# Kernel optimization log

Hardware: AMD Instinct MI355X
Metric: run time of the kernel (lower is better)

The kernel has to match this reference:

```python
import jax, jax.numpy as jnp
import numpy as np

B, S, HID = 2, 2048, 1024
NH, NKV, HD = 16, 8, 128
EPS = 1e-6
THETA = 1.0e6
NEG = -1e9

def _rope_tables():
    inv_freq = 1.0 / (THETA ** (np.arange(0, HD, 2, dtype=np.float32) / HD))  # [HD/2]
    pos = np.arange(S, dtype=np.float32)
    freqs = np.outer(pos, inv_freq)                      # [S, HD/2]
    emb = np.concatenate([freqs, freqs], axis=-1)        # [S, HD]
    cos = np.broadcast_to(np.cos(emb), (B, S, HD)).copy()
    sin = np.broadcast_to(np.sin(emb), (B, S, HD)).copy()
    return jnp.asarray(cos), jnp.asarray(sin)

def setup_inputs() -> dict:
    key = jax.random.key(0)
    ks = jax.random.split(key, 8)
    hidden_states = jax.random.normal(ks[0], (B, S, HID), jnp.float32)
    cos, sin = _rope_tables()
    # additive causal mask [B,1,S,S]
    causal = jnp.triu(jnp.full((S, S), NEG, jnp.float32), k=1)
    attention_mask = jnp.broadcast_to(causal[None, None], (B, 1, S, S))
    std = 0.02
    Wq = jax.random.normal(ks[1], (NH * HD, HID), jnp.float32) * std
    Wk = jax.random.normal(ks[2], (NKV * HD, HID), jnp.float32) * std
    Wv = jax.random.normal(ks[3], (NKV * HD, HID), jnp.float32) * std
    Wo = jax.random.normal(ks[4], (HID, NH * HD), jnp.float32) * std
    q_norm_w = jnp.ones((HD,), jnp.float32)
    k_norm_w = jnp.ones((HD,), jnp.float32)
    return {"hidden_states": hidden_states, "cos": cos, "sin": sin,
            "attention_mask": attention_mask, "Wq": Wq, "Wk": Wk, "Wv": Wv,
            "Wo": Wo, "q_norm_w": q_norm_w, "k_norm_w": k_norm_w}

def _rms_norm(x, w):
    var = jnp.mean(jnp.square(x), axis=-1, keepdims=True)
    return x * jax.lax.rsqrt(var + EPS) * w

def _rotate_half(x):
    x1, x2 = jnp.split(x, 2, axis=-1)
    return jnp.concatenate([-x2, x1], axis=-1)

def reference(hidden_states, cos, sin, attention_mask, Wq, Wk, Wv, Wo, q_norm_w, k_norm_w):
    # projections: [B,S,heads,HD] -> [B,heads,S,HD]
    q = jnp.einsum('bsh,dh->bsd', hidden_states, Wq).reshape(B, S, NH, HD)
    k = jnp.einsum('bsh,dh->bsd', hidden_states, Wk).reshape(B, S, NKV, HD)
    v = jnp.einsum('bsh,dh->bsd', hidden_states, Wv).reshape(B, S, NKV, HD)
    q = jnp.transpose(_rms_norm(q, q_norm_w), (0, 2, 1, 3))
    k = jnp.transpose(_rms_norm(k, k_norm_w), (0, 2, 1, 3))
    v = jnp.transpose(v, (0, 2, 1, 3))
    c = cos[:, None]  # [B,1,S,HD]
    s = sin[:, None]
    q = q * c + _rotate_half(q) * s
    k = k * c + _rotate_half(k) * s
    # repeat kv heads: NKV -> NH
    n_rep = NH // NKV
    k = jnp.repeat(k, n_rep, axis=1)
    v = jnp.repeat(v, n_rep, axis=1)
    scaling = HD ** -0.5
    scores = jnp.einsum('bhqd,bhkd->bhqk', q, k) * scaling
    scores = scores + attention_mask
    probs = jax.nn.softmax(scores.astype(jnp.float32), axis=-1).astype(q.dtype)
    out = jnp.einsum('bhqk,bhkd->bhqd', probs, v)
    out = jnp.transpose(out, (0, 2, 1, 3)).reshape(B, S, NH * HD)
    return jnp.einsum('bsd,hd->bsh', out, Wo)
```

## Files before the change

### kernel.cpp

```cpp
#include <hip/hip_runtime.h>
#include <hip/hip_fp16.h>


typedef _Float16 f16;
typedef __attribute__((ext_vector_type(8))) _Float16 f16x8;
typedef __attribute__((ext_vector_type(4))) _Float16 f16x4;
typedef __attribute__((ext_vector_type(4))) float f32x4;

__constant__ const float kEps = 1e-6f;
__constant__ const float kScaleL2 = 0.1275179120685481f;

#define ASYNC_LD16(gp, lp)                                              \
  __builtin_amdgcn_global_load_lds(                                     \
      (const __attribute__((address_space(1))) void*)(gp),              \
      (__attribute__((address_space(3))) void*)(uint32_t)(uintptr_t)(lp), 16, 0, 0)

__global__ __launch_bounds__(256) void cast_all(
    const float* __restrict__ h, const float* __restrict__ wq,
    const float* __restrict__ wk, const float* __restrict__ wv,
    const float* __restrict__ wo, f16* __restrict__ hb,
    f16* __restrict__ wqkv, f16* __restrict__ wob) {
  const int idx = blockIdx.x * 256 + threadIdx.x;
  const float* src;
  f16* dst;
  int base;
  if (idx < 1048576) { src = h;  dst = hb;                  base = 0; }
  else if (idx < 1572864) { src = wq; dst = wqkv;               base = 1048576; }
  else if (idx < 1835008) { src = wk; dst = wqkv + 2048 * 1024; base = 1572864; }
  else if (idx < 2097152) { src = wv; dst = wqkv + 3072 * 1024; base = 1835008; }
  else { src = wo; dst = wob; base = 2097152; }
  const int i = (idx - base) * 4;
  f32x4 v = *reinterpret_cast<const f32x4*>(src + i);
  f16x4 o;
  o.x = (f16)v.x; o.y = (f16)v.y; o.z = (f16)v.z; o.w = (f16)v.w;
  *reinterpret_cast<f16x4*>(dst + i) = o;
}

__global__ __launch_bounds__(256) void gemm_bt_h(const f16* __restrict__ A,
                                                 const f16* __restrict__ Bm,
                                                 f16* __restrict__ C,
                                                 int M, int N, int K) {
  __shared__ __align__(16) f16 As[128][64];
  __shared__ __align__(16) f16 Bs[128][64];
  const int tid = threadIdx.x;
  const int lane = tid & 63;
  const int wave = tid >> 6;
  const int cl = lane & 15;
  const int quad = lane >> 4;
  const int wm = (wave >> 1) * 64;
  const int wn = (wave & 1) * 64;
  const int tm = blockIdx.y * 128;
  const int tn = blockIdx.x * 128;
  const int r0 = tid >> 3;
  const int csw = ((tid & 7) ^ (r0 & 7)) * 8;

  const f16* Ab = A + (size_t)(tm + r0) * K + csw;
  const f16* Bb = Bm + (size_t)(tn + r0) * K + csw;
  char* Al = (char*)As + wave * 1024;
  char* Bl = (char*)Bs + wave * 1024;

  f32x4 acc[4][4] = {};

  for (int k0 = 0; k0 < K; k0 += 64) {
#pragma unroll
    for (int c = 0; c < 4; ++c) {
      ASYNC_LD16(Ab + (size_t)(c * 32) * K + k0, Al + c * 4096);
      ASYNC_LD16(Bb + (size_t)(c * 32) * K + k0, Bl + c * 4096);
    }
    __syncthreads();
#pragma unroll
    for (int kk = 0; kk < 2; ++kk) {
      f16x8 af[4], bf[4];
#pragma unroll
      for (int mi = 0; mi < 4; ++mi)
        af[mi] = *reinterpret_cast<const f16x8*>(
            &As[wm + mi * 16 + cl][((kk * 4 + quad) ^ (cl & 7)) * 8]);
#pragma unroll
      for (int ni = 0; ni < 4; ++ni)
        bf[ni] = *reinterpret_cast<const f16x8*>(
            &Bs[wn + ni * 16 + cl][((kk * 4 + quad) ^ (cl & 7)) * 8]);
#pragma unroll
      for (int mi = 0; mi < 4; ++mi)
#pragma unroll
        for (int ni = 0; ni < 4; ++ni)
          acc[mi][ni] =
              __builtin_amdgcn_mfma_f32_16x16x32_f16(af[mi], bf[ni], acc[mi][ni], 0, 0, 0);
    }
    __syncthreads();
  }
#pragma unroll
  for (int mi = 0; mi < 4; ++mi)
#pragma unroll
    for (int ni = 0; ni < 4; ++ni)
#pragma unroll
      for (int r = 0; r < 4; ++r)
        C[(size_t)(tm + wm + mi * 16 + quad * 4 + r) * N + tn + wn + ni * 16 + cl] =
            (f16)acc[mi][ni][r];
}

__global__ __launch_bounds__(256) void gemm_bt64(const f16* __restrict__ A,
                                                 const f16* __restrict__ Bm,
                                                 float* __restrict__ C,
                                                 int M, int N, int K) {
  __shared__ __align__(16) f16 As[64][64];
  __shared__ __align__(16) f16 Bs[128][64];
  const int tid = threadIdx.x;
  const int lane = tid & 63;
  const int wave = tid >> 6;
  const int cl = lane & 15;
  const int quad = lane >> 4;
  const int wm = (wave >> 1) * 32;
  const int wn = (wave & 1) * 64;
  const int tm = blockIdx.y * 64;
  const int tn = blockIdx.x * 128;
  const int r0 = tid >> 3;
  const int csw = ((tid & 7) ^ (r0 & 7)) * 8;

  const f16* Ab = A + (size_t)(tm + r0) * K + csw;
  const f16* Bb = Bm + (size_t)(tn + r0) * K + csw;
  char* Al = (char*)As + wave * 1024;
  char* Bl = (char*)Bs + wave * 1024;

  f32x4 acc[2][4] = {};

  for (int k0 = 0; k0 < K; k0 += 64) {
#pragma unroll
    for (int c = 0; c < 2; ++c)
      ASYNC_LD16(Ab + (size_t)(c * 32) * K + k0, Al + c * 4096);
#pragma unroll
    for (int c = 0; c < 4; ++c)
      ASYNC_LD16(Bb + (size_t)(c * 32) * K + k0, Bl + c * 4096);
    __syncthreads();
#pragma unroll
    for (int kk = 0; kk < 2; ++kk) {
      f16x8 af[2], bf[4];
#pragma unroll
      for (int mi = 0; mi < 2; ++mi)
        af[mi] = *reinterpret_cast<const f16x8*>(
            &As[wm + mi * 16 + cl][((kk * 4 + quad) ^ (cl & 7)) * 8]);
#pragma unroll
      for (int ni = 0; ni < 4; ++ni)
        bf[ni] = *reinterpret_cast<const f16x8*>(
            &Bs[wn + ni * 16 + cl][((kk * 4 + quad) ^ (cl & 7)) * 8]);
#pragma unroll
      for (int mi = 0; mi < 2; ++mi)
#pragma unroll
        for (int ni = 0; ni < 4; ++ni)
          acc[mi][ni] =
              __builtin_amdgcn_mfma_f32_16x16x32_f16(af[mi], bf[ni], acc[mi][ni], 0, 0, 0);
    }
    __syncthreads();
  }
#pragma unroll
  for (int mi = 0; mi < 2; ++mi)
#pragma unroll
    for (int ni = 0; ni < 4; ++ni)
#pragma unroll
      for (int r = 0; r < 4; ++r)
        C[(size_t)(tm + wm + mi * 16 + quad * 4 + r) * N + tn + wn + ni * 16 + cl] =
            acc[mi][ni][r];
}

__global__ __launch_bounds__(256) void rope_norm(
    const f16* __restrict__ qkvh,
    const float* __restrict__ cosT, const float* __restrict__ sinT,
    const float* __restrict__ qw, const float* __restrict__ kw,
    f16* __restrict__ qt, f16* __restrict__ kt) {
  const int gw = blockIdx.x * 4 + (threadIdx.x >> 6);
  const int lane = threadIdx.x & 63;
  const int head = gw % 24;
  const int bs = gw / 24;
  const bool isq = head < 16;
  const f16* src = qkvh + (size_t)bs * 4096 +
                   (isq ? head * 128 : 2048 + (head - 16) * 128);
  const float x1 = (float)src[lane];
  const float x2 = (float)src[lane + 64];
  float ss = x1 * x1 + x2 * x2;
#pragma unroll
  for (int off = 32; off >= 1; off >>= 1) ss += __shfl_xor(ss, off);
  const float rms = rsqrtf(ss * (1.0f / 128.0f) + kEps);
  const float* w = isq ? qw : kw;
  const float n1 = x1 * rms * w[lane];
  const float n2 = x2 * rms * w[lane + 64];
  const float* cb = cosT + (size_t)bs * 128;
  const float* sb = sinT + (size_t)bs * 128;
  const float o1 = n1 * cb[lane] - n2 * sb[lane];
  const float o2 = n2 * cb[lane + 64] + n1 * sb[lane + 64];
  const int b = bs >> 11;
  const int s = bs & 2047;
  f16* dst;
  float sc;
  if (isq) {
    dst = qt + ((size_t)(b * 16 + head) * 2048 + s) * 128;
    sc = kScaleL2;
  } else {
    dst = kt + ((size_t)(b * 8 + (head - 16)) * 2048 + s) * 128;
    sc = 1.0f;
  }
  dst[lane] = (f16)(o1 * sc);
  dst[lane + 64] = (f16)(o2 * sc);
}

__global__ __launch_bounds__(256) void v_transpose(const f16* __restrict__ qkvh,
                                                   f16* __restrict__ vt) {
  __shared__ __align__(16) f16 tile[64][136];
  const int bh = blockIdx.y;
  const int b = bh >> 3, h = bh & 7;
  const int s0 = blockIdx.x * 64;
  const int tid = threadIdx.x;
#pragma unroll
  for (int i = 0; i < 4; ++i) {
    int c = tid + i * 256;
    int s = c >> 4;
    int cg = c & 15;
    f16x8 v = *reinterpret_cast<const f16x8*>(
        qkvh + (size_t)(b * 2048 + s0 + s) * 4096 + 3072 + h * 128 + cg * 8);
    *reinterpret_cast<f16x8*>(&tile[s][cg * 8]) = v;
  }
  __syncthreads();
#pragma unroll
  for (int i = 0; i < 4; ++i) {
    int c = tid + i * 256;
    int d = c >> 3;
    int sB = (c & 7) * 8;
    f16x8 o;
#pragma unroll
    for (int j = 0; j < 8; ++j) o[j] = tile[sB + j][d];
    *reinterpret_cast<f16x8*>(vt + ((size_t)(b * 8 + h) * 128 + d) * 2048 + s0 + sB) = o;
  }
}

__global__ __launch_bounds__(128) void attn(const f16* __restrict__ Qt,
                                            const f16* __restrict__ Kt,
                                            const f16* __restrict__ Vt,
                                            f16* __restrict__ Ot) {
  __shared__ __align__(16) f16 Ks[64 * 128];
  __shared__ __align__(16) f16 Vs[128 * 64];
  __shared__ __align__(16) f16 Ps[2][32][72];

  const int bid = blockIdx.x;
  const int bh = bid & 31;
  const int t = 31 - (bid >> 5);
  const int q0 = t * 64;
  const int b = bh >> 4, h = bh & 15;
  const int kv = h >> 1;

  const int tid = threadIdx.x;
  const int lane = tid & 63, wv = tid >> 6;
  const int cl = lane & 15, quad = lane >> 4;
  const int qw0 = q0 + wv * 32;

  const f16* qbase = Qt + ((size_t)(b * 16 + h) * 2048 + qw0 + cl) * 128;
  f16x8 aq[2][4];
#pragma unroll
  for (int mi = 0; mi < 2; ++mi)
#pragma unroll
    for (int kk = 0; kk < 4; ++kk)
      aq[mi][kk] =
          *reinterpret_cast<const f16x8*>(qbase + mi * 16 * 128 + kk * 32 + quad * 8);

  const f16* kbase = Kt + (size_t)(b * 8 + kv) * 2048 * 128;
  const f16* vbase = Vt + (size_t)(b * 8 + kv) * 128 * 2048;

  float m_[2] = {-1e30f, -1e30f}, l_[2] = {0.f, 0.f};
  f32x4 oacc[2][8] = {};

  for (int kt0 = 0; kt0 <= q0; kt0 += 64) {
#pragma unroll
    for (int i = 0; i < 8; ++i) {
      const int c = (wv * 8 + i) * 64 + lane;
      const int kr = c >> 4, kg = c & 15;
      const int kgs = (kg & 8) | ((kg & 7) ^ (kr & 7));
      ASYNC_LD16(kbase + (size_t)(kt0 + kr) * 128 + kgs * 8,
                 (char*)Ks + (wv * 8 + i) * 1024);
      const int vr = c >> 3, vg = c & 7;
      const int vgs = vg ^ (vr & 7);
      ASYNC_LD16(vbase + (size_t)vr * 2048 + kt0 + vgs * 8,
                 (char*)Vs + (wv * 8 + i) * 1024);
    }
    __syncthreads();
    f32x4 sacc[2][4] = {};
#pragma unroll
    for (int kk = 0; kk < 4; ++kk)
#pragma unroll
      for (int ni = 0; ni < 4; ++ni) {
        const int gk = kk * 4 + quad;
        const int gks = (gk & 8) | ((gk & 7) ^ (cl & 7));
        f16x8 ak =
            *reinterpret_cast<const f16x8*>(Ks + (ni * 16 + cl) * 128 + gks * 8);
#pragma unroll
        for (int mi = 0; mi < 2; ++mi)
          sacc[mi][ni] =
              __builtin_amdgcn_mfma_f32_16x16x32_f16(ak, aq[mi][kk], sacc[mi][ni], 0, 0, 0);
      }
    if (kt0 == q0) {
#pragma unroll
      for (int mi = 0; mi < 2; ++mi) {
        const int qg = qw0 + mi * 16 + cl;
#pragma unroll
        for (int ni = 0; ni < 4; ++ni) {
          const int sg = kt0 + ni * 16 + quad * 4;
#pragma unroll
          for (int r = 0; r < 4; ++r)
            if (sg + r > qg) sacc[mi][ni][r] = -1e30f;
        }
      }
    }
    float al[2];
#pragma unroll
    for (int mi = 0; mi < 2; ++mi) {
      float m0 = sacc[mi][0][0];
#pragma unroll
      for (int ni = 0; ni < 4; ++ni)
#pragma unroll
        for (int r = 0; r < 4; ++r) m0 = fmaxf(m0, sacc[mi][ni][r]);
      m0 = fmaxf(m0, __shfl_xor(m0, 16));
      m0 = fmaxf(m0, __shfl_xor(m0, 32));
      const float nm = fmaxf(m_[mi], m0);
      al[mi] = __builtin_amdgcn_exp2f(m_[mi] - nm);
      m_[mi] = nm;
      float ps = 0.f;
#pragma unroll
      for (int ni = 0; ni < 4; ++ni)
#pragma unroll
        for (int r = 0; r < 4; ++r) {
          const float p = __builtin_amdgcn_exp2f(sacc[mi][ni][r] - nm);
          sacc[mi][ni][r] = p;
          ps += p;
        }
      l_[mi] = l_[mi] * al[mi] + ps;
    }
#pragma unroll
    for (int mi = 0; mi < 2; ++mi)
#pragma unroll
      for (int ni = 0; ni < 4; ++ni) {
        f16x4 pk;
#pragma unroll
        for (int r = 0; r < 4; ++r) pk[r] = (f16)sacc[mi][ni][r];
        *reinterpret_cast<f16x4*>(&Ps[wv][mi * 16 + cl][ni * 16 + quad * 4]) = pk;
      }
#pragma unroll
    for (int mi = 0; mi < 2; ++mi)
#pragma unroll
      for (int dg = 0; dg < 8; ++dg) oacc[mi][dg] *= al[mi];
    asm volatile("s_waitcnt lgkmcnt(0)" ::: "memory");
    f16x8 bp[2][2];
#pragma unroll
    for (int mi = 0; mi < 2; ++mi)
#pragma unroll
      for (int kh = 0; kh < 2; ++kh)
        bp[mi][kh] =
            *reinterpret_cast<const f16x8*>(&Ps[wv][mi * 16 + cl][kh * 32 + quad * 8]);
#pragma unroll
    for (int kh = 0; kh < 2; ++kh)
#pragma unroll
      for (int dg = 0; dg < 8; ++dg) {
        const int gv = kh * 4 + quad;
        const int gvs = gv ^ (cl & 7);
        f16x8 av =
            *reinterpret_cast<const f16x8*>(Vs + (dg * 16 + cl) * 64 + gvs * 8);
#pragma unroll
        for (int mi = 0; mi < 2; ++mi)
          oacc[mi][dg] =
              __builtin_amdgcn_mfma_f32_16x16x32_f16(av, bp[mi][kh], oacc[mi][dg], 0, 0, 0);
      }
    __syncthreads();
  }
#pragma unroll
  for (int mi = 0; mi < 2; ++mi) {
    float l = l_[mi];
    l += __shfl_xor(l, 16);
    l += __shfl_xor(l, 32);
    const float inv = 1.0f / l;
    const size_t qg = qw0 + mi * 16 + cl;
#pragma unroll
    for (int dg = 0; dg < 8; ++dg) {
      f16x4 o;
#pragma unroll
      for (int r = 0; r < 4; ++r) o[r] = (f16)(oacc[mi][dg][r] * inv);
      *reinterpret_cast<f16x4*>(Ot + ((size_t)b * 2048 + qg) * 2048 + h * 128 +
                                dg * 16 + quad * 4) = o;
    }
  }
}

extern "C" void kernel_launch(void* const* d_in, const int* in_sizes, int n_in,
                              void* d_out, int out_size, void* d_ws, size_t ws_size,
                              hipStream_t stream) {
  (void)in_sizes; (void)n_in; (void)out_size; (void)ws_size;
  const float* hidden = (const float*)d_in[0];
  const float* cosT = (const float*)d_in[1];
  const float* sinT = (const float*)d_in[2];
  const float* Wq = (const float*)d_in[4];
  const float* Wk = (const float*)d_in[5];
  const float* Wv = (const float*)d_in[6];
  const float* Wo = (const float*)d_in[7];
  const float* qnw = (const float*)d_in[8];
  const float* knw = (const float*)d_in[9];
  float* out = (float*)d_out;

  char* ws = (char*)d_ws;
  size_t off = 0;
  auto alloc = [&](size_t bytes) {
    char* p = ws + off;
    off += (bytes + 255) & ~(size_t)255;
    return p;
  };
  f16* hb = (f16*)alloc(4096ull * 1024 * 2);
  f16* wqkv = (f16*)alloc(4096ull * 1024 * 2);
  f16* wob = (f16*)alloc(1024ull * 2048 * 2);
  f16* qkvh = (f16*)alloc(4096ull * 4096 * 2);
  f16* qt = (f16*)alloc(32ull * 2048 * 128 * 2);
  f16* kt = (f16*)alloc(16ull * 2048 * 128 * 2);
  f16* vt = (f16*)alloc(16ull * 2048 * 128 * 2);
  f16* ot = (f16*)alloc(4096ull * 2048 * 2);

  cast_all<<<10240, 256, 0, stream>>>(hidden, Wq, Wk, Wv, Wo, hb, wqkv, wob);

  gemm_bt_h<<<dim3(32, 32), 256, 0, stream>>>(hb, wqkv, qkvh, 4096, 4096, 1024);

  rope_norm<<<24576, 256, 0, stream>>>(qkvh, cosT, sinT, qnw, knw, qt, kt);
  v_transpose<<<dim3(32, 16), 256, 0, stream>>>(qkvh, vt);

  attn<<<1024, 128, 0, stream>>>(qt, kt, vt, ot);

  gemm_bt64<<<dim3(8, 64), 256, 0, stream>>>(ot, wob, out, 4096, 1024, 2048);
}
```

Baseline: 302.6 us.

## Split attention KV tile across four waves with split-K softmax merge

The attention kernel goes from 2 to 4 waves per block. Each pair of waves shares a 32-row query slice and splits each 64-key tile into two 32-key halves, keeping separate running max/sum and output accumulators. The halves are merged at the end through shared memory using the log-sum-exp rescale. Fully masked halves are skipped, and s_setprio is raised around the MFMA sections. The aim is more waves in flight per CU to hide latency and less wasted work on the diagonal tile, at the cost of an extra merge step, an extra barrier and more shared-memory traffic.

```diff
diff --git a/kernel.cpp b/kernel.cpp
--- a/kernel.cpp
+++ b/kernel.cpp
@@ -230,13 +230,13 @@
   }
 }
 
-__global__ __launch_bounds__(128) void attn(const f16* __restrict__ Qt,
-                                            const f16* __restrict__ Kt,
-                                            const f16* __restrict__ Vt,
-                                            f16* __restrict__ Ot) {
+__global__ __launch_bounds__(256, 3) void attn(const f16* __restrict__ Qt,
+                                               const f16* __restrict__ Kt,
+                                               const f16* __restrict__ Vt,
+                                               f16* __restrict__ Ot) {
   __shared__ __align__(16) f16 Ks[64 * 128];
   __shared__ __align__(16) f16 Vs[128 * 64];
-  __shared__ __align__(16) f16 Ps[2][32][72];
+  __shared__ __align__(16) f16 Ps[4][32][40];
 
   const int bid = blockIdx.x;
   const int bh = bid & 31;
@@ -248,7 +248,9 @@
   const int tid = threadIdx.x;
   const int lane = tid & 63, wv = tid >> 6;
   const int cl = lane & 15, quad = lane >> 4;
-  const int qw0 = q0 + wv * 32;
+  const int qh = wv & 1;
+  const int sh = wv >> 1;
+  const int qw0 = q0 + qh * 32;
 
   const f16* qbase = Qt + ((size_t)(b * 16 + h) * 2048 + qw0 + cl) * 128;
   f16x8 aq[2][4];
@@ -257,7 +259,7 @@
 #pragma unroll
     for (int kk = 0; kk < 4; ++kk)
       aq[mi][kk] =
-          *reinterpret_cast<const f16x8*>(qbase + mi * 16 * 128 + kk * 32 + quad * 8);
+          *reinterpret_cast<const f16x8*>(qbase + mi * 2048 + kk * 32 + quad * 8);
 
   const f16* kbase = Kt + (size_t)(b * 8 + kv) * 2048 * 128;
   const f16* vbase = Vt + (size_t)(b * 8 + kv) * 128 * 2048;
@@ -267,119 +269,149 @@
 
   for (int kt0 = 0; kt0 <= q0; kt0 += 64) {
 #pragma unroll
-    for (int i = 0; i < 8; ++i) {
-      const int c = (wv * 8 + i) * 64 + lane;
+    for (int i = 0; i < 4; ++i) {
+      const int c = i * 256 + tid;
       const int kr = c >> 4, kg = c & 15;
       const int kgs = (kg & 8) | ((kg & 7) ^ (kr & 7));
       ASYNC_LD16(kbase + (size_t)(kt0 + kr) * 128 + kgs * 8,
-                 (char*)Ks + (wv * 8 + i) * 1024);
+                 (char*)Ks + i * 4096 + wv * 1024);
       const int vr = c >> 3, vg = c & 7;
       const int vgs = vg ^ (vr & 7);
       ASYNC_LD16(vbase + (size_t)vr * 2048 + kt0 + vgs * 8,
-                 (char*)Vs + (wv * 8 + i) * 1024);
-    }
-    __syncthreads();
-    f32x4 sacc[2][4] = {};
-#pragma unroll
-    for (int kk = 0; kk < 4; ++kk)
-#pragma unroll
-      for (int ni = 0; ni < 4; ++ni) {
+                 (char*)Vs + i * 4096 + wv * 1024);
+    }
+    __syncthreads();
+    if (kt0 + sh * 32 <= qw0 + 31) {
+      f32x4 sacc[2][2] = {};
+      __builtin_amdgcn_s_setprio(1);
+#pragma unroll
+      for (int kk = 0; kk < 4; ++kk) {
         const int gk = kk * 4 + quad;
         const int gks = (gk & 8) | ((gk & 7) ^ (cl & 7));
-        f16x8 ak =
-            *reinterpret_cast<const f16x8*>(Ks + (ni * 16 + cl) * 128 + gks * 8);
-#pragma unroll
-        for (int mi = 0; mi < 2; ++mi)
-          sacc[mi][ni] =
-              __builtin_amdgcn_mfma_f32_16x16x32_f16(ak, aq[mi][kk], sacc[mi][ni], 0, 0, 0);
-      }
-    if (kt0 == q0) {
+#pragma unroll
+        for (int ni = 0; ni < 2; ++ni) {
+          f16x8 ak = *reinterpret_cast<const f16x8*>(
+              Ks + (sh * 32 + ni * 16 + cl) * 128 + gks * 8);
+#pragma unroll
+          for (int mi = 0; mi < 2; ++mi)
+            sacc[mi][ni] =
+                __builtin_amdgcn_mfma_f32_16x16x32_f16(ak, aq[mi][kk], sacc[mi][ni], 0, 0, 0);
+        }
+      }
+      __builtin_amdgcn_s_setprio(0);
+      if (kt0 + sh * 32 + 31 > qw0) {
+#pragma unroll
+        for (int mi = 0; mi < 2; ++mi) {
+          const int qg = qw0 + mi * 16 + cl;
+#pragma unroll
+          for (int ni = 0; ni < 2; ++ni) {
+            const int sg = kt0 + sh * 32 + ni * 16 + quad * 4;
+#pragma unroll
+            for (int r = 0; r < 4; ++r)
+              if (sg + r > qg) sacc[mi][ni][r] = -1e30f;
+          }
+        }
+      }
+      float al[2];
 #pragma unroll
       for (int mi = 0; mi < 2; ++mi) {
-        const int qg = qw0 + mi * 16 + cl;
-#pragma unroll
-        for (int ni = 0; ni < 4; ++ni) {
-          const int sg = kt0 + ni * 16 + quad * 4;
-#pragma unroll
-          for (int r = 0; r < 4; ++r)
-            if (sg + r > qg) sacc[mi][ni][r] = -1e30f;
+        float m0 = sacc[mi][0][0];
+#pragma unroll
+        for (int ni = 0; ni < 2; ++ni)
+#pragma unroll
+          for (int r = 0; r < 4; ++r) m0 = fmaxf(m0, sacc[mi][ni][r]);
+        m0 = fmaxf(m0, __shfl_xor(m0, 16));
+        m0 = fmaxf(m0, __shfl_xor(m0, 32));
+        const float nm = fmaxf(m_[mi], m0);
+        al[mi] = __builtin_amdgcn_exp2f(m_[mi] - nm);
+        m_[mi] = nm;
+        float ps = 0.f;
+#pragma unroll
+        for (int ni = 0; ni < 2; ++ni)
+#pragma unroll
+          for (int r = 0; r < 4; ++r) {
+            const float p = __builtin_amdgcn_exp2f(sacc[mi][ni][r] - nm);
+            sacc[mi][ni][r] = p;
+            ps += p;
+          }
+        l_[mi] = l_[mi] * al[mi] + ps;
+      }
+#pragma unroll
+      for (int mi = 0; mi < 2; ++mi)
+#pragma unroll
+        for (int ni = 0; ni < 2; ++ni) {
+          f16x4 pk;
+#pragma unroll
+          for (int r = 0; r < 4; ++r) pk[r] = (f16)sacc[mi][ni][r];
+          *reinterpret_cast<f16x4*>(&Ps[wv][mi * 16 + cl][ni * 16 + quad * 4]) = pk;
         }
-      }
-    }
-    float al[2];
-#pragma unroll
-    for (int mi = 0; mi < 2; ++mi) {
-      float m0 = sacc[mi][0][0];
-#pragma unroll
-      for (int ni = 0; ni < 4; ++ni)
-#pragma unroll
-        for (int r = 0; r < 4; ++r) m0 = fmaxf(m0, sacc[mi][ni][r]);
-      m0 = fmaxf(m0, __shfl_xor(m0, 16));
-      m0 = fmaxf(m0, __shfl_xor(m0, 32));
-      const float nm = fmaxf(m_[mi], m0);
-      al[mi] = __builtin_amdgcn_exp2f(m_[mi] - nm);
-      m_[mi] = nm;
-      float ps = 0.f;
-#pragma unroll
-      for (int ni = 0; ni < 4; ++ni)
-#pragma unroll
-        for (int r = 0; r < 4; ++r) {
-          const float p = __builtin_amdgcn_exp2f(sacc[mi][ni][r] - nm);
-          sacc[mi][ni][r] = p;
-          ps += p;
-        }
-      l_[mi] = l_[mi] * al[mi] + ps;
-    }
-#pragma unroll
-    for (int mi = 0; mi < 2; ++mi)
-#pragma unroll
-      for (int ni = 0; ni < 4; ++ni) {
-        f16x4 pk;
-#pragma unroll
-        for (int r = 0; r < 4; ++r) pk[r] = (f16)sacc[mi][ni][r];
-        *reinterpret_cast<f16x4*>(&Ps[wv][mi * 16 + cl][ni * 16 + quad * 4]) = pk;
-      }
-#pragma unroll
-    for (int mi = 0; mi < 2; ++mi)
-#pragma unroll
-      for (int dg = 0; dg < 8; ++dg) oacc[mi][dg] *= al[mi];
-    asm volatile("s_waitcnt lgkmcnt(0)" ::: "memory");
-    f16x8 bp[2][2];
-#pragma unroll
-    for (int mi = 0; mi < 2; ++mi)
-#pragma unroll
-      for (int kh = 0; kh < 2; ++kh)
-        bp[mi][kh] =
-            *reinterpret_cast<const f16x8*>(&Ps[wv][mi * 16 + cl][kh * 32 + quad * 8]);
-#pragma unroll
-    for (int kh = 0; kh < 2; ++kh)
+#pragma unroll
+      for (int mi = 0; mi < 2; ++mi)
+#pragma unroll
+        for (int dg = 0; dg < 8; ++dg) oacc[mi][dg] *= al[mi];
+      asm volatile("s_waitcnt lgkmcnt(0)" ::: "memory");
+      f16x8 bp[2];
+#pragma unroll
+      for (int mi = 0; mi < 2; ++mi)
+        bp[mi] = *reinterpret_cast<const f16x8*>(&Ps[wv][mi * 16 + cl][quad * 8]);
+      __builtin_amdgcn_s_setprio(1);
 #pragma unroll
       for (int dg = 0; dg < 8; ++dg) {
-        const int gv = kh * 4 + quad;
+        const int gv = sh * 4 + quad;
         const int gvs = gv ^ (cl & 7);
         f16x8 av =
             *reinterpret_cast<const f16x8*>(Vs + (dg * 16 + cl) * 64 + gvs * 8);
 #pragma unroll
         for (int mi = 0; mi < 2; ++mi)
           oacc[mi][dg] =
-              __builtin_amdgcn_mfma_f32_16x16x32_f16(av, bp[mi][kh], oacc[mi][dg], 0, 0, 0);
-      }
-    __syncthreads();
-  }
-#pragma unroll
-  for (int mi = 0; mi < 2; ++mi) {
-    float l = l_[mi];
-    l += __shfl_xor(l, 16);
-    l += __shfl_xor(l, 32);
-    const float inv = 1.0f / l;
-    const size_t qg = qw0 + mi * 16 + cl;
-#pragma unroll
-    for (int dg = 0; dg < 8; ++dg) {
-      f16x4 o;
-#pragma unroll
-      for (int r = 0; r < 4; ++r) o[r] = (f16)(oacc[mi][dg][r] * inv);
-      *reinterpret_cast<f16x4*>(Ot + ((size_t)b * 2048 + qg) * 2048 + h * 128 +
-                                dg * 16 + quad * 4) = o;
+              __builtin_amdgcn_mfma_f32_16x16x32_f16(av, bp[mi], oacc[mi][dg], 0, 0, 0);
+      }
+      __builtin_amdgcn_s_setprio(0);
+    }
+    __syncthreads();
+  }
+  float* xo = (qh == 0) ? (float*)Ks : (float*)Vs;
+  float* xml = (float*)&Ps[0][0][0] + qh * 256;
+  if (sh == 1) {
+#pragma unroll
+    for (int mi = 0; mi < 2; ++mi)
+#pragma unroll
+      for (int dg = 0; dg < 8; ++dg) {
+        const int idx = mi * 8 + dg;
+        *reinterpret_cast<f32x4*>(xo + lane * 64 + ((idx ^ (lane & 7)) << 2)) =
+            oacc[mi][dg];
+      }
+    xml[lane * 4 + 0] = m_[0];
+    xml[lane * 4 + 1] = m_[1];
+    xml[lane * 4 + 2] = l_[0];
+    xml[lane * 4 + 3] = l_[1];
+  }
+  __syncthreads();
+  if (sh == 0) {
+#pragma unroll
+    for (int mi = 0; mi < 2; ++mi) {
+      const float m2 = xml[lane * 4 + mi];
+      const float l2 = xml[lane * 4 + 2 + mi];
+      const float nm = fmaxf(m_[mi], m2);
+      const float a1 = __builtin_amdgcn_exp2f(m_[mi] - nm);
+      const float a2 = __builtin_amdgcn_exp2f(m2 - nm);
+      float lm = l_[mi] * a1 + l2 * a2;
+      lm += __shfl_xor(lm, 16);
+      lm += __shfl_xor(lm, 32);
+      const float inv = 1.0f / lm;
+      const size_t qg = qw0 + mi * 16 + cl;
+#pragma unroll
+      for (int dg = 0; dg < 8; ++dg) {
+        const int idx = mi * 8 + dg;
+        f32x4 o2 = *reinterpret_cast<const f32x4*>(
+            xo + lane * 64 + ((idx ^ (lane & 7)) << 2));
+        f16x4 o;
+#pragma unroll
+        for (int r = 0; r < 4; ++r)
+          o[r] = (f16)((oacc[mi][dg][r] * a1 + o2[r] * a2) * inv);
+        *reinterpret_cast<f16x4*>(Ot + ((size_t)b * 2048 + qg) * 2048 + h * 128 +
+                                  dg * 16 + quad * 4) = o;
+      }
     }
   }
 }
@@ -422,7 +454,7 @@
   rope_norm<<<24576, 256, 0, stream>>>(qkvh, cosT, sinT, qnw, knw, qt, kt);
   v_transpose<<<dim3(32, 16), 256, 0, stream>>>(qkvh, vt);
 
-  attn<<<1024, 128, 0, stream>>>(qt, kt, vt, ot);
+  attn<<<1024, 256, 0, stream>>>(qt, kt, vt, ot);
 
   gemm_bt64<<<dim3(8, 64), 256, 0, stream>>>(ot, wob, out, 4096, 1024, 2048);
 }
```

New measurement: 288.1 us. 4.8% less time.
